# Kernel tuning notes

Measured on AMD Instinct MI355X. Metric: run time of the kernel, lower is better.

The kernel has to match this reference:

```python
import jax, jax.numpy as jnp
import numpy as np

N_NODES = 50000
N_EDGES = 800000
IN_CH = 256
HID_CH = 128


def setup_inputs() -> dict:
    key = jax.random.key(0)
    k1, k2, k3, k4, k5 = jax.random.split(key, 5)
    x = jax.random.normal(k1, (N_NODES, IN_CH), dtype=jnp.float32)
    edge_index = jax.random.randint(k2, (2, N_EDGES), 0, N_NODES, dtype=jnp.int64)
    edge_weight = jax.random.uniform(k3, (N_EDGES,), dtype=jnp.float32)
    W = jax.random.normal(k4, (IN_CH, HID_CH), dtype=jnp.float32) * (1.0 / np.sqrt(IN_CH))
    b = jnp.zeros((HID_CH,), dtype=jnp.float32)
    alpha = jnp.full((HID_CH,), 0.25, dtype=jnp.float32)  # PReLU default init
    return {"x": x, "edge_index": edge_index, "edge_weight": edge_weight,
            "W": W, "b": b, "alpha": alpha}


def reference(x, edge_index, edge_weight, W, b, alpha):
    """GCNConv (with self-loops + symmetric normalization) followed by PReLU."""
    N = x.shape[0]
    row, col = edge_index[0], edge_index[1]
    # add self-loops with weight 1 (PyG gcn_norm default, add_self_loops=True)
    loop = jnp.arange(N, dtype=row.dtype)
    row = jnp.concatenate([row, loop])
    col = jnp.concatenate([col, loop])
    ew = jnp.concatenate([edge_weight, jnp.ones((N,), dtype=edge_weight.dtype)])
    # degree from edge weights, scattered at destination (col)
    deg = jax.ops.segment_sum(ew, col, num_segments=N)
    deg_inv_sqrt = jnp.where(deg > 0, jax.lax.rsqrt(deg), 0.0)
    norm = deg_inv_sqrt[row] * ew * deg_inv_sqrt[col]  # [E+N]
    # linear transform then gather-scale-scatter aggregation
    h = x @ W                               # [N, HID]
    msg = h[row] * norm[:, None]            # [E+N, HID]
    out = jax.ops.segment_sum(msg, col, num_segments=N) + b
    # PReLU with per-channel slope
    return jnp.where(out >= 0, out, alpha * out)
```

## Files before the change

### kernel.cpp

```cpp
#include <hip/hip_runtime.h>

#define NN 50000
#define NE 800000
#define KD 256
#define CD 128
#define NB 196
#define GEMM_BLOCKS 782
#define HIST_BLOCKS 3125
#define META_BLOCKS 782

typedef __attribute__((ext_vector_type(8))) short short8;
typedef __attribute__((ext_vector_type(4))) float floatx4;
typedef __attribute__((ext_vector_type(2))) float floatx2;

__device__ inline unsigned short f2bf(float f) {
    unsigned u = __float_as_uint(f);
    unsigned r = (u + 0x7FFFu + ((u >> 16) & 1u)) >> 16;
    return (unsigned short)r;
}
__device__ inline float bf2f_lo(unsigned u) { return __uint_as_float(u << 16); }
__device__ inline float bf2f_hi(unsigned u) { return __uint_as_float(u & 0xFFFF0000u); }

__global__ __launch_bounds__(256) void prep(const float* __restrict__ W,
                                            unsigned short* __restrict__ Wt,
                                            unsigned* __restrict__ packedAll,
                                            unsigned long long* __restrict__ state) {
    __shared__ unsigned short t[32][33];
    if (blockIdx.x < NB) {
        const int g = blockIdx.x * 256 + threadIdx.x;
        if (g < NN) {
#pragma unroll
            for (int c = 0; c < 4; c++) packedAll[(size_t)c * NN + g] = 0u;
        }
        if (blockIdx.x == 0) {
            for (int i = threadIdx.x; i < NB * 8; i += 256) state[i] = 0ull;
        }
        return;
    }
    const int b2 = blockIdx.x - NB;
    const int bk = (b2 & 7) * 32;
    const int bn = (b2 >> 3) * 32;
    const int tx = threadIdx.x & 31;
    const int ty = threadIdx.x >> 5;
#pragma unroll
    for (int i = 0; i < 32; i += 8)
        t[ty + i][tx] = f2bf(W[(size_t)(bk + ty + i) * CD + bn + tx]);
    __syncthreads();
#pragma unroll
    for (int i = 0; i < 32; i += 8)
        Wt[(size_t)(bn + ty + i) * KD + bk + tx] = t[tx][ty + i];
}

__global__ __launch_bounds__(256) void fused_gemm_hist(
        const float* __restrict__ x, const unsigned short* __restrict__ Wt,
        unsigned short* __restrict__ hb,
        const int* __restrict__ col, const float* __restrict__ ew,
        unsigned* __restrict__ packedAll, unsigned short* __restrict__ rank) {
    __shared__ unsigned short As[64][40];
    __shared__ unsigned short Bs[128][40];

    if (blockIdx.x >= GEMM_BLOCKS) {
        const int hblk = blockIdx.x - GEMM_BLOCKS;
        const int e = hblk * 256 + threadIdx.x;
        if (e < NE) {
            unsigned* packed = packedAll + (size_t)(hblk & 3) * NN;
            unsigned p = (1u << 24) + (unsigned)(ew[e] * 262144.0f);
            unsigned old = atomicAdd(&packed[col[e]], p);
            rank[e] = (unsigned short)(old >> 24);
        }
        return;
    }

    const int tid  = threadIdx.x;
    const int wave = tid >> 6;
    const int lane = tid & 63;
    const int row0 = blockIdx.x * 64;
    const int m0   = wave * 16;
    const int lr   = lane & 15;
    const int quad = lane >> 4;

    const int ar = tid >> 2;
    const int aq = tid & 3;
    const int bn = tid >> 1;
    const int bh = (tid & 1) * 16;

    const int gr = row0 + ar;
    const bool ok = gr < NN;
    const float* xb = x + (size_t)gr * KD + aq * 8;
    const unsigned short* wb = Wt + (size_t)bn * KD + bh;

    floatx4 acc[8];
#pragma unroll
    for (int nt = 0; nt < 8; nt++) acc[nt] = (floatx4){0.f, 0.f, 0.f, 0.f};

    float4 f0 = {0.f, 0.f, 0.f, 0.f}, f1 = {0.f, 0.f, 0.f, 0.f};
    short8 wv0, wv1;
    if (ok) { f0 = *(const float4*)xb; f1 = *(const float4*)(xb + 4); }
    wv0 = *(const short8*)wb;
    wv1 = *(const short8*)(wb + 8);

#pragma unroll
    for (int kt = 0; kt < 8; kt++) {
        union { short8 v; unsigned short us[8]; } av;
        if (ok) {
            av.us[0] = f2bf(f0.x); av.us[1] = f2bf(f0.y);
            av.us[2] = f2bf(f0.z); av.us[3] = f2bf(f0.w);
            av.us[4] = f2bf(f1.x); av.us[5] = f2bf(f1.y);
            av.us[6] = f2bf(f1.z); av.us[7] = f2bf(f1.w);
        } else {
            av.v = (short8){0,0,0,0,0,0,0,0};
        }
        *(short8*)&As[ar][aq * 8] = av.v;
        *(short8*)&Bs[bn][bh]     = wv0;
        *(short8*)&Bs[bn][bh + 8] = wv1;
        __syncthreads();
        if (kt < 7) {
            const float* xp = xb + (kt + 1) * 32;
            if (ok) { f0 = *(const float4*)xp; f1 = *(const float4*)(xp + 4); }
            const unsigned short* wp = wb + (kt + 1) * 32;
            wv0 = *(const short8*)wp;
            wv1 = *(const short8*)(wp + 8);
        }
        short8 af = *(const short8*)&As[m0 + lr][quad * 8];
#pragma unroll
        for (int nt = 0; nt < 8; nt++) {
            short8 bfr = *(const short8*)&Bs[nt * 16 + lr][quad * 8];
            acc[nt] = __builtin_amdgcn_mfma_f32_16x16x32_bf16(af, bfr, acc[nt], 0, 0, 0);
        }
        __syncthreads();
    }

#pragma unroll
    for (int i = 0; i < 4; i++) {
        const int grow = row0 + m0 + quad * 4 + i;
        if (grow < NN) {
            unsigned short* hp = hb + (size_t)grow * CD + lr;
#pragma unroll
            for (int nt = 0; nt < 8; nt++)
                hp[nt * 16] = f2bf(acc[nt][i]);
        }
    }
}

__global__ __launch_bounds__(256) void scan_lookback(
        const unsigned* __restrict__ packedAll,
        unsigned long long* __restrict__ state,
        int* __restrict__ start, int4* __restrict__ base4,
        float* __restrict__ dinv) {
    __shared__ int sm[256];
    __shared__ int sbase;
    const int t = threadIdx.x;
    const int b = blockIdx.x;
    const int g = b * 256 + t;

    int cc[4] = {0, 0, 0, 0};
    unsigned lowsum = 0;
    int v = 0;
    if (g < NN) {
#pragma unroll
        for (int c = 0; c < 4; c++) {
            unsigned p = packedAll[(size_t)c * NN + g];
            cc[c] = (int)(p >> 24);
            lowsum += p & 0xFFFFFFu;
            v += cc[c];
        }
    }
    sm[t] = v;
    __syncthreads();
#pragma unroll
    for (int off = 1; off < 256; off <<= 1) {
        int u = (t >= off) ? sm[t - off] : 0;
        __syncthreads();
        sm[t] += u;
        __syncthreads();
    }
    const int incl = sm[t];
    const int total = sm[255];

    if (t == 0) {
        unsigned long long post =
            ((b == 0 ? 2ull : 1ull) << 32) | (unsigned)total;
        __hip_atomic_store(&state[(size_t)b * 8], post,
                           __ATOMIC_RELAXED, __HIP_MEMORY_SCOPE_AGENT);
        if (b == 0) sbase = 0;
    }
    if (b > 0 && t < 64) {
        long long run = 0;
        int i = b - 1;
        while (true) {
            const int idx = i - t;
            unsigned long long s = (idx >= 0)
                ? __hip_atomic_load(&state[(size_t)idx * 8],
                                    __ATOMIC_RELAXED, __HIP_MEMORY_SCOPE_AGENT)
                : (2ull << 32);
            const unsigned st = (unsigned)(s >> 32);
            const unsigned long long b0m = __ballot(st == 0u);
            const unsigned long long b2m = __ballot(st == 2u);
            if (b2m) {
                const int L = __ffsll((long long)b2m) - 1;
                const unsigned long long below =
                    (L == 63) ? ~0ull : ((1ull << (L + 1)) - 1ull);
                if (b0m & below) { __builtin_amdgcn_s_sleep(1); continue; }
                unsigned val = (t <= L) ? (unsigned)s : 0u;
#pragma unroll
                for (int o = 32; o; o >>= 1) val += __shfl_xor(val, o);
                run += val;
                break;
            } else if (b0m) {
                const int L0 = __ffsll((long long)b0m) - 1;
                unsigned val = (t < L0) ? (unsigned)s : 0u;
#pragma unroll
                for (int o = 32; o; o >>= 1) val += __shfl_xor(val, o);
                run += val;
                i -= L0;
                if (L0 == 0) __builtin_amdgcn_s_sleep(1);
            } else {
                unsigned val = (unsigned)s;
#pragma unroll
                for (int o = 32; o; o >>= 1) val += __shfl_xor(val, o);
                run += val;
                i -= 64;
            }
        }
        if (t == 0) {
            __hip_atomic_store(&state[(size_t)b * 8],
                               (2ull << 32) | (unsigned)(run + total),
                               __ATOMIC_RELAXED, __HIP_MEMORY_SCOPE_AGENT);
            sbase = (int)run;
        }
    }
    __syncthreads();
    const int base = sbase;

    if (g < NN) {
        const int s = base + (incl - v);
        start[g] = s;
        base4[g] = make_int4(s, s + cc[0], s + cc[0] + cc[1], s + cc[0] + cc[1] + cc[2]);
        float degs = (float)lowsum * (1.0f / 262144.0f);
        dinv[g] = rsqrtf(1.0f + degs);
    }
    if (g == 0) start[NN] = NE;
}

__global__ __launch_bounds__(256) void meta_write(const int* __restrict__ row,
                                                  const int* __restrict__ col,
                                                  const float* __restrict__ ew,
                                                  const unsigned short* __restrict__ rank,
                                                  const int4* __restrict__ base4,
                                                  const float* __restrict__ dinv,
                                                  unsigned* __restrict__ meta) {
    const int e0 = (blockIdx.x * 256 + threadIdx.x) * 4;
    if (e0 >= NE) return;
    const int4 c4 = *(const int4*)(col + e0);
    const int4 r4 = *(const int4*)(row + e0);
    const float4 w4 = *(const float4*)(ew + e0);
    const ushort4 k4 = *(const ushort4*)(rank + e0);
    const int cs[4] = {c4.x, c4.y, c4.z, c4.w};
    const int rs[4] = {r4.x, r4.y, r4.z, r4.w};
    const float wsv[4] = {w4.x, w4.y, w4.z, w4.w};
    const unsigned short ks[4] = {k4.x, k4.y, k4.z, k4.w};
#pragma unroll
    for (int j = 0; j < 4; j++) {
        const int e = e0 + j;
        const int copy = (e >> 8) & 3;
        const int4 b4 = base4[cs[j]];
        const int base = (copy == 0) ? b4.x : (copy == 1) ? b4.y
                       : (copy == 2) ? b4.z : b4.w;
        const unsigned short wbf = f2bf(dinv[rs[j]] * wsv[j]);
        meta[base + ks[j]] = ((unsigned)wbf << 16) | (unsigned)rs[j];
    }
}

__global__ __launch_bounds__(256) void aggregate(const int* __restrict__ start,
                                                 const unsigned* __restrict__ meta,
                                                 const unsigned short* __restrict__ hb,
                                                 const float* __restrict__ dinv,
                                                 const float* __restrict__ bias,
                                                 const float* __restrict__ alpha,
                                                 float* __restrict__ out) {
    int n = blockIdx.x * 4 + (threadIdx.x >> 6);
    if (n >= NN) return;
    n = __builtin_amdgcn_readfirstlane(n);
    const int lane = threadIdx.x & 63;
    const int s = __builtin_amdgcn_readfirstlane(start[n]);
    const int e = __builtin_amdgcn_readfirstlane(start[n + 1]);

    float A0[8], A1[8];
#pragma unroll
    for (int j = 0; j < 8; j++) { A0[j] = 0.f; A1[j] = 0.f; }

    int i = s;
    for (; i + 8 <= e; i += 8) {
        unsigned m[8], u[8];
#pragma unroll
        for (int j = 0; j < 8; j++) m[j] = __builtin_nontemporal_load(meta + i + j);
#pragma unroll
        for (int j = 0; j < 8; j++)
            u[j] = *(const unsigned*)(hb + (size_t)(m[j] & 0xFFFFu) * CD + lane * 2);
#pragma unroll
        for (int j = 0; j < 8; j++) {
            float w = __uint_as_float(m[j] & 0xFFFF0000u);
            A0[j] = fmaf(w, bf2f_lo(u[j]), A0[j]);
            A1[j] = fmaf(w, bf2f_hi(u[j]), A1[j]);
        }
    }
    for (; i < e; i++) {
        unsigned m = __builtin_nontemporal_load(meta + i);
        unsigned u = *(const unsigned*)(hb + (size_t)(m & 0xFFFFu) * CD + lane * 2);
        float w = __uint_as_float(m & 0xFFFF0000u);
        A0[0] = fmaf(w, bf2f_lo(u), A0[0]);
        A1[0] = fmaf(w, bf2f_hi(u), A1[0]);
    }
#pragma unroll
    for (int j = 1; j < 8; j++) { A0[0] += A0[j]; A1[0] += A1[j]; }

    const float dc = dinv[n];
    unsigned us = *(const unsigned*)(hb + (size_t)n * CD + lane * 2);
    const int ch = lane * 2;
    float o0 = dc * A0[0] + dc * dc * bf2f_lo(us) + bias[ch];
    float o1 = dc * A1[0] + dc * dc * bf2f_hi(us) + bias[ch + 1];
    o0 = o0 >= 0.f ? o0 : alpha[ch] * o0;
    o1 = o1 >= 0.f ? o1 : alpha[ch + 1] * o1;
    floatx2 o; o.x = o0; o.y = o1;
    __builtin_nontemporal_store(o, (floatx2*)(out + (size_t)n * CD + ch));
}

extern "C" void kernel_launch(void* const* d_in, const int* in_sizes, int n_in,
                              void* d_out, int out_size, void* d_ws, size_t ws_size,
                              hipStream_t stream) {
    const float* x     = (const float*)d_in[0];
    const int*   eidx  = (const int*)d_in[1];
    const float* ew    = (const float*)d_in[2];
    const float* Wm    = (const float*)d_in[3];
    const float* bias  = (const float*)d_in[4];
    const float* alpha = (const float*)d_in[5];
    const int* row = eidx;
    const int* col = eidx + NE;

    float* out = (float*)d_out;

    char* ws = (char*)d_ws;
    unsigned* packedAll = (unsigned*)(ws);
    int*   start    = (int*)(ws + 800000);
    float* dinv     = (float*)(ws + 1000064);
    unsigned short* rank = (unsigned short*)(ws + 1200064);
    int4*  base4    = (int4*)(ws + 2800064);
    unsigned* meta  = (unsigned*)(ws + 3600064);
    unsigned short* Wt = (unsigned short*)(ws + 6800064);
    unsigned long long* state = (unsigned long long*)(ws + 6865600);
    unsigned short* hb = (unsigned short*)(ws + 6878208);

    prep          <<<NB + 32, 256, 0, stream>>>(Wm, Wt, packedAll, state);
    fused_gemm_hist<<<GEMM_BLOCKS + HIST_BLOCKS, 256, 0, stream>>>(
                        x, Wt, hb, col, ew, packedAll, rank);
    scan_lookback <<<NB, 256, 0, stream>>>(packedAll, state, start, base4, dinv);
    meta_write    <<<META_BLOCKS, 256, 0, stream>>>(row, col, ew, rank, base4, dinv, meta);
    aggregate     <<<(NN + 3) / 4, 256, 0, stream>>>(start, meta, hb, dinv, bias, alpha, out);
}
```

Baseline: 186.2 us.

## Drop LDS staging in GEMM and vectorize histogram to four edges per thread

The GEMM part now loads A fragments and W fragments straight from global memory into MFMA registers. This removes the shared-memory tiles and both __syncthreads per k-step, at the cost of redundant W reads across waves, which should mostly be served from cache. The histogram blocks now process four edges per thread with vector loads of col and ew and a vector store of ranks, cutting the block count by four. The histogram copy index now comes from the wave id instead of the block id. This changes which edges share a copy of packedAll, so the rank values change, but each copy still receives an exact count.

```diff
diff --git a/kernel.cpp b/kernel.cpp
--- a/kernel.cpp
+++ b/kernel.cpp
@@ -6,7 +6,7 @@
 #define CD 128
 #define NB 196
 #define GEMM_BLOCKS 782
-#define HIST_BLOCKS 3125
+#define HIST4_BLOCKS 782
 #define META_BLOCKS 782
 
 typedef __attribute__((ext_vector_type(8))) short short8;
@@ -56,17 +56,22 @@
         unsigned short* __restrict__ hb,
         const int* __restrict__ col, const float* __restrict__ ew,
         unsigned* __restrict__ packedAll, unsigned short* __restrict__ rank) {
-    __shared__ unsigned short As[64][40];
-    __shared__ unsigned short Bs[128][40];
-
     if (blockIdx.x >= GEMM_BLOCKS) {
-        const int hblk = blockIdx.x - GEMM_BLOCKS;
-        const int e = hblk * 256 + threadIdx.x;
-        if (e < NE) {
-            unsigned* packed = packedAll + (size_t)(hblk & 3) * NN;
-            unsigned p = (1u << 24) + (unsigned)(ew[e] * 262144.0f);
-            unsigned old = atomicAdd(&packed[col[e]], p);
-            rank[e] = (unsigned short)(old >> 24);
+        const int e0 = ((blockIdx.x - GEMM_BLOCKS) * 256 + threadIdx.x) * 4;
+        if (e0 < NE) {
+            const int4 c4 = *(const int4*)(col + e0);
+            const float4 w4 = *(const float4*)(ew + e0);
+            unsigned* packed = packedAll + (size_t)((threadIdx.x >> 6) & 3) * NN;
+            const unsigned o0 = atomicAdd(&packed[c4.x], (1u << 24) + (unsigned)(w4.x * 262144.0f));
+            const unsigned o1 = atomicAdd(&packed[c4.y], (1u << 24) + (unsigned)(w4.y * 262144.0f));
+            const unsigned o2 = atomicAdd(&packed[c4.z], (1u << 24) + (unsigned)(w4.z * 262144.0f));
+            const unsigned o3 = atomicAdd(&packed[c4.w], (1u << 24) + (unsigned)(w4.w * 262144.0f));
+            ushort4 r;
+            r.x = (unsigned short)(o0 >> 24);
+            r.y = (unsigned short)(o1 >> 24);
+            r.z = (unsigned short)(o2 >> 24);
+            r.w = (unsigned short)(o3 >> 24);
+            *(ushort4*)(rank + e0) = r;
         }
         return;
     }
@@ -79,30 +84,21 @@
     const int lr   = lane & 15;
     const int quad = lane >> 4;
 
-    const int ar = tid >> 2;
-    const int aq = tid & 3;
-    const int bn = tid >> 1;
-    const int bh = (tid & 1) * 16;
-
-    const int gr = row0 + ar;
-    const bool ok = gr < NN;
-    const float* xb = x + (size_t)gr * KD + aq * 8;
-    const unsigned short* wb = Wt + (size_t)bn * KD + bh;
+    const int grow_a = row0 + m0 + lr;
+    const bool ok = grow_a < NN;
+    const float* xp = x + (size_t)grow_a * KD + quad * 8;
+    const unsigned short* wp = Wt + (size_t)lr * KD + quad * 8;
 
     floatx4 acc[8];
 #pragma unroll
     for (int nt = 0; nt < 8; nt++) acc[nt] = (floatx4){0.f, 0.f, 0.f, 0.f};
 
-    float4 f0 = {0.f, 0.f, 0.f, 0.f}, f1 = {0.f, 0.f, 0.f, 0.f};
-    short8 wv0, wv1;
-    if (ok) { f0 = *(const float4*)xb; f1 = *(const float4*)(xb + 4); }
-    wv0 = *(const short8*)wb;
-    wv1 = *(const short8*)(wb + 8);
-
-#pragma unroll
+#pragma unroll 2
     for (int kt = 0; kt < 8; kt++) {
         union { short8 v; unsigned short us[8]; } av;
         if (ok) {
+            const float4 f0 = *(const float4*)(xp + kt * 32);
+            const float4 f1 = *(const float4*)(xp + kt * 32 + 4);
             av.us[0] = f2bf(f0.x); av.us[1] = f2bf(f0.y);
             av.us[2] = f2bf(f0.z); av.us[3] = f2bf(f0.w);
             av.us[4] = f2bf(f1.x); av.us[5] = f2bf(f1.y);
@@ -110,24 +106,13 @@
         } else {
             av.v = (short8){0,0,0,0,0,0,0,0};
         }
-        *(short8*)&As[ar][aq * 8] = av.v;
-        *(short8*)&Bs[bn][bh]     = wv0;
-        *(short8*)&Bs[bn][bh + 8] = wv1;
-        __syncthreads();
-        if (kt < 7) {
-            const float* xp = xb + (kt + 1) * 32;
-            if (ok) { f0 = *(const float4*)xp; f1 = *(const float4*)(xp + 4); }
-            const unsigned short* wp = wb + (kt + 1) * 32;
-            wv0 = *(const short8*)wp;
-            wv1 = *(const short8*)(wp + 8);
-        }
-        short8 af = *(const short8*)&As[m0 + lr][quad * 8];
-#pragma unroll
-        for (int nt = 0; nt < 8; nt++) {
-            short8 bfr = *(const short8*)&Bs[nt * 16 + lr][quad * 8];
-            acc[nt] = __builtin_amdgcn_mfma_f32_16x16x32_bf16(af, bfr, acc[nt], 0, 0, 0);
-        }
-        __syncthreads();
+        short8 b[8];
+#pragma unroll
+        for (int nt = 0; nt < 8; nt++)
+            b[nt] = *(const short8*)(wp + (size_t)nt * 16 * KD + kt * 32);
+#pragma unroll
+        for (int nt = 0; nt < 8; nt++)
+            acc[nt] = __builtin_amdgcn_mfma_f32_16x16x32_bf16(av.v, b[nt], acc[nt], 0, 0, 0);
     }
 
 #pragma unroll
@@ -351,7 +336,7 @@
     unsigned short* hb = (unsigned short*)(ws + 6878208);
 
     prep          <<<NB + 32, 256, 0, stream>>>(Wm, Wt, packedAll, state);
-    fused_gemm_hist<<<GEMM_BLOCKS + HIST_BLOCKS, 256, 0, stream>>>(
+    fused_gemm_hist<<<GEMM_BLOCKS + HIST4_BLOCKS, 256, 0, stream>>>(
                         x, Wt, hb, col, ew, packedAll, rank);
     scan_lookback <<<NB, 256, 0, stream>>>(packedAll, state, start, base4, dinv);
     meta_write    <<<META_BLOCKS, 256, 0, stream>>>(row, col, ew, rank, base4, dinv, meta);
```

Result: slower. 209.9 us (+12.8%).
